# Kernel optimization log

Measured on AMD Instinct MI355X. Metric: run time of the kernel, lower is better.

Reference implementation:

```python
import jax, jax.numpy as jnp
import numpy as np
import math

B, S, D, H = 2, 2048, 1024, 16
DK = D // H
EPS = 1e-5

def setup_inputs() -> dict:
    key = jax.random.key(0)
    ks = jax.random.split(key, 16)
    s = 0.02
    return {
        'query': jax.random.normal(ks[0], (B, S, D), jnp.float32),
        'key': jax.random.normal(ks[1], (B, S, D), jnp.float32),
        'value': jax.random.normal(ks[2], (B, S, D), jnp.float32),
        'mask': jax.random.randint(ks[3], (B, 1, S, S), 0, 2, jnp.int32),
        'market_context': jax.random.normal(ks[4], (B, D), jnp.float32),
        'Wq': jax.random.normal(ks[5], (D, D), jnp.float32) * s,
        'bq': jnp.zeros((D,), jnp.float32),
        'Wk': jax.random.normal(ks[6], (D, D), jnp.float32) * s,
        'bk': jnp.zeros((D,), jnp.float32),
        'Wv': jax.random.normal(ks[7], (D, D), jnp.float32) * s,
        'bv': jnp.zeros((D,), jnp.float32),
        'Wo': jax.random.normal(ks[8], (D, D), jnp.float32) * s,
        'bo': jnp.zeros((D,), jnp.float32),
        'Wc': jax.random.normal(ks[9], (D, D), jnp.float32) * s,
        'bc': jnp.zeros((D,), jnp.float32),
        'ln_g': jnp.ones((D,), jnp.float32),
        'ln_b': jnp.zeros((D,), jnp.float32),
    }

def reference(query, key, value, mask, market_context,
              Wq, bq, Wk, bk, Wv, bv, Wo, bo, Wc, bc, ln_g, ln_b):
    b, s, d = query.shape
    # QKV projections -> [B, H, S, DK]
    Q = (query @ Wq + bq).reshape(b, s, H, DK).transpose(0, 2, 1, 3)
    K = (key @ Wk + bk).reshape(b, s, H, DK).transpose(0, 2, 1, 3)
    V = (value @ Wv + bv).reshape(b, s, H, DK).transpose(0, 2, 1, 3)
    # market context -> per-head bias added to K (broadcast over sequence)
    ctx = (market_context @ Wc + bc).reshape(b, H, DK)
    K = K + ctx[:, :, None, :]
    scores = jnp.einsum('bhqd,bhkd->bhqk', Q, K) / math.sqrt(DK)
    scores = jnp.where(mask == 0, jnp.float32(-1e9), scores)
    attn = jax.nn.softmax(scores, axis=-1)  # dropout is identity in eval
    ctx2 = jnp.einsum('bhqk,bhkd->bhqd', attn, V)
    ctx2 = ctx2.transpose(0, 2, 1, 3).reshape(b, s, d)
    out = ctx2 @ Wo + bo
    x = out + query
    mu = jnp.mean(x, axis=-1, keepdims=True)
    var = jnp.mean((x - mu) ** 2, axis=-1, keepdims=True)
    return (x - mu) * jax.lax.rsqrt(var + EPS) * ln_g + ln_b
```

## Files before the change

### kernel.cpp

```cpp
#include <hip/hip_runtime.h>
#include <cstdint>

typedef unsigned short u16;
typedef __attribute__((ext_vector_type(8))) short s16x8;
typedef __attribute__((ext_vector_type(8))) unsigned short u16x8;
typedef __attribute__((ext_vector_type(4))) float f32x4;
typedef __attribute__((ext_vector_type(16))) float f32x16;
typedef __attribute__((ext_vector_type(2))) unsigned uint2v;
typedef __attribute__((ext_vector_type(4))) unsigned uint4v;

#define CKF 0.18033688011f

__device__ inline u16 f2bf(float f){
  union { float f; uint32_t u; } v; v.f = f;
  uint32_t r = v.u + 0x7fffu + ((v.u >> 16) & 1u);
  return (u16)(r >> 16);
}

__device__ inline f32x4 mfma16(s16x8 a, s16x8 b, f32x4 c){
  return __builtin_amdgcn_mfma_f32_16x16x32_bf16(a, b, c, 0, 0, 0);
}
__device__ inline f32x16 mfma32(s16x8 a, s16x8 b, f32x16 c){
  return __builtin_amdgcn_mfma_f32_32x32x16_bf16(a, b, c, 0, 0, 0);
}
__device__ inline unsigned cvtpk(float a, float b){
  unsigned r;
  asm("v_cvt_pk_bf16_f32 %0, %1, %2" : "=v"(r) : "v"(a), "v"(b));
  return r;
}
__device__ inline float exp2a(float x){
  float r;
  asm("v_exp_f32 %0, %1" : "=v"(r) : "v"(x));
  return r;
}
__device__ inline void glds16(const u16* g, u16* l){
  __builtin_amdgcn_global_load_lds((const __attribute__((address_space(1))) void*)g,
                                   (__attribute__((address_space(3))) void*)l, 16, 0, 0);
}
__device__ inline void glds4(const unsigned* g, unsigned* l){
  __builtin_amdgcn_global_load_lds((const __attribute__((address_space(1))) void*)g,
                                   (__attribute__((address_space(3))) void*)l, 4, 0, 0);
}

struct PrepParams {
  const float* q; const float* k; const float* v;
  const int* mask; const float* mc;
  const float* W0; const float* W1; const float* W2; const float* W3;
  const float* Wc;
  u16* qo; u16* ko; u16* vo;
  u16* T0; u16* T1; u16* T2; u16* T3;
  unsigned* bits; float* part;
};

__global__ __launch_bounds__(256) void prep_kernel(PrepParams PP){
  __shared__ float shf[1056];
  int blk = blockIdx.x, tid = threadIdx.x;
  if (blk < 6144){
    int byy = blk >> 11, bxx = blk & 2047;
    const float* src = (byy == 0) ? PP.q : (byy == 1) ? PP.k : PP.v;
    u16* dst = (byy == 0) ? PP.qo : (byy == 1) ? PP.ko : PP.vo;
    size_t i = ((size_t)bxx * 256 + tid) * 8;
    float4 a = *(const float4*)(src + i);
    float4 b = *(const float4*)(src + i + 4);
    u16x8 o = { f2bf(a.x), f2bf(a.y), f2bf(a.z), f2bf(a.w),
                f2bf(b.x), f2bf(b.y), f2bf(b.z), f2bf(b.w) };
    *(u16x8*)(dst + i) = o;
  } else if (blk < 10240){
    int idx = blk - 6144;
    int bxx = idx & 31, byy = (idx >> 5) & 31, bzz = idx >> 10;
    const float* W = (bzz == 0) ? PP.W0 : (bzz == 1) ? PP.W1 : (bzz == 2) ? PP.W2 : PP.W3;
    u16* T = (bzz == 0) ? PP.T0 : (bzz == 1) ? PP.T1 : (bzz == 2) ? PP.T2 : PP.T3;
    float (*t)[33] = (float(*)[33])shf;
    int n0 = bxx * 32, k0 = byy * 32;
    int tx = tid & 31, ty = tid >> 5;
    #pragma unroll
    for (int j = 0; j < 4; j++)
      t[ty + j*8][tx] = W[(size_t)(k0 + ty + j*8) * 1024 + n0 + tx];
    __syncthreads();
    #pragma unroll
    for (int j = 0; j < 4; j++)
      T[(size_t)(n0 + ty + j*8) * 1024 + k0 + tx] = f2bf(t[tx][ty + j*8]);
  } else if (blk < 43008){
    size_t i = (size_t)(blk - 10240) * 256 + tid;
    int v = PP.mask[i];
    unsigned long long bal = __ballot(v != 0);
    int lane = tid & 63;
    if (lane == 0)       PP.bits[i >> 5] = (unsigned)bal;
    else if (lane == 32) PP.bits[i >> 5] = (unsigned)(bal >> 32);
  } else {
    int slice = blk - 43008;
    int k0 = slice * 64;
    float4 a0 = {0.f,0.f,0.f,0.f}, a1 = {0.f,0.f,0.f,0.f};
    const float* wp = PP.Wc + (size_t)k0 * 1024 + tid * 4;
    #pragma unroll 8
    for (int k = 0; k < 64; k++){
      float4 wv = *(const float4*)(wp + (size_t)k * 1024);
      float m0 = PP.mc[k0 + k], m1 = PP.mc[1024 + k0 + k];
      a0.x += m0 * wv.x; a0.y += m0 * wv.y; a0.z += m0 * wv.z; a0.w += m0 * wv.w;
      a1.x += m1 * wv.x; a1.y += m1 * wv.y; a1.z += m1 * wv.z; a1.w += m1 * wv.w;
    }
    *(float4*)(PP.part + ((size_t)slice * 2 + 0) * 1024 + tid * 4) = a0;
    *(float4*)(PP.part + ((size_t)slice * 2 + 1) * 1024 + tid * 4) = a1;
  }
}

__global__ __launch_bounds__(256) void ctxred_kernel(const float* __restrict__ part,
                                                     const float* __restrict__ bc,
                                                     float* __restrict__ ctx){
  int b = blockIdx.x, tid = threadIdx.x;
  float4 s = *(const float4*)(bc + tid * 4);
  #pragma unroll 4
  for (int sl = 0; sl < 16; sl++){
    float4 p = *(const float4*)(part + ((size_t)sl * 2 + b) * 1024 + tid * 4);
    s.x += p.x; s.y += p.y; s.z += p.z; s.w += p.w;
  }
  *(float4*)(ctx + (size_t)b * 1024 + tid * 4) = s;
}

struct GemmParams {
  const u16* A0; const u16* A1; const u16* A2; const u16* A3;
  const u16* W0; const u16* W1; const u16* W2; const u16* W3;
  const float* b0; const float* b1; const float* b2;
  const float* ctx;
  u16* outQ; u16* outK; u16* outV; float* outX0; float* outX1;
  int which;
};

__global__ __launch_bounds__(256) void gemm_kernel(GemmParams P){
  int o = blockIdx.x + (blockIdx.y << 3) + (blockIdx.z << 8);
  int xcd = o & 7, j = o >> 3;
  int by = xcd + ((j & 3) << 3);
  int bx = (j >> 2) & 7;
  int bz = j >> 5;

  int z, kbase, nkt;
  const u16* A; const u16* W;
  if (P.which < 0){
    z = bz; kbase = 0; nkt = 32;
    if (z == 0){ A = P.A0; W = P.W0; }
    else if (z == 1){ A = P.A1; W = P.W1; }
    else { A = P.A2; W = P.W2; }
  } else {
    z = 3; kbase = bz * 512; nkt = 16;
    A = P.A3; W = P.W3;
  }
  int m0 = by * 128, n0 = bx * 128;
  __shared__ __align__(16) u16 sm[16384];
  int tid = threadIdx.x, lane = tid & 63, w = tid >> 6;
  int li = lane & 15, lq = lane >> 4;
  int wm = w >> 1, wn = w & 1;
  f32x4 zero = {0.f, 0.f, 0.f, 0.f};
  f32x4 acc[4][4];
  #pragma unroll
  for (int i = 0; i < 4; i++)
    #pragma unroll
    for (int jj = 0; jj < 4; jj++) acc[i][jj] = zero;

  int scolS = ((lane & 3) ^ ((lane >> 3) & 3)) << 3;
  int row0 = w * 16 + (lane >> 2);
  const u16* aS0 = A + (size_t)(m0 + row0) * 1024 + kbase + scolS;
  const u16* aS1 = aS0 + (size_t)64 * 1024;
  const u16* bS0 = W + (size_t)(n0 + row0) * 1024 + kbase + scolS;
  const u16* bS1 = bS0 + (size_t)64 * 1024;
  int aD0 = (w * 64) * 8, aD1 = (256 + w * 64) * 8;

  int aOff[4], bOff[4];
  #pragma unroll
  for (int mb = 0; mb < 4; mb++){
    int row = wm * 64 + mb * 16 + li;
    aOff[mb] = (row * 32 + ((lq ^ ((row >> 1) & 3)) << 3)) * 2;
  }
  #pragma unroll
  for (int nb = 0; nb < 4; nb++){
    int row = wn * 64 + nb * 16 + li;
    bOff[nb] = 8192 + (row * 32 + ((lq ^ ((row >> 1) & 3)) << 3)) * 2;
  }

  auto STAGE = [&](int ct){
    u16* Ab = &sm[ct * 8192];
    u16* Bb = &sm[ct * 8192 + 4096];
    glds16(aS0, Ab + aD0);
    glds16(aS1, Ab + aD1);
    glds16(bS0, Bb + aD0);
    glds16(bS1, Bb + aD1);
  };
  auto ADV = [&](){ aS0 += 32; aS1 += 32; bS0 += 32; bS1 += 32; };

  auto KITER = [&](int kt, int ct){
    __builtin_amdgcn_s_barrier();
    if (kt + 1 < nkt){
      STAGE(ct ^ 1); ADV();
      asm volatile("s_waitcnt vmcnt(4)" ::: "memory");
    } else {
      asm volatile("s_waitcnt vmcnt(0)" ::: "memory");
    }
    __builtin_amdgcn_sched_barrier(0);
    __builtin_amdgcn_s_barrier();
    const char* base = (const char*)sm + ct * 16384;
    s16x8 af[4], bfr[4];
    #pragma unroll
    for (int mb = 0; mb < 4; mb++) af[mb] = *(const s16x8*)(base + aOff[mb]);
    #pragma unroll
    for (int nb = 0; nb < 4; nb++) bfr[nb] = *(const s16x8*)(base + bOff[nb]);
    __builtin_amdgcn_s_setprio(1);
    #pragma unroll
    for (int mb = 0; mb < 4; mb++)
      #pragma unroll
      for (int nb = 0; nb < 4; nb++)
        acc[mb][nb] = mfma16(af[mb], bfr[nb], acc[mb][nb]);
    __builtin_amdgcn_s_setprio(0);
  };

  STAGE(0); ADV();
  for (int kt = 0; kt < nkt; kt += 2){
    KITER(kt, 0);
    KITER(kt + 1, 1);
  }

  if (z == 2){
    const float* bias = P.b2;
    __syncthreads();
    u16* Ot = sm;
    #pragma unroll
    for (int mb = 0; mb < 4; mb++){
      #pragma unroll
      for (int nb = 0; nb < 4; nb++){
        int colL = wn * 64 + nb * 16 + li;
        int rowB = wm * 64 + mb * 16 + lq * 4;
        float bcol = bias[n0 + colL];
        unsigned p01 = cvtpk(acc[mb][nb][0] + bcol, acc[mb][nb][1] + bcol);
        unsigned p23 = cvtpk(acc[mb][nb][2] + bcol, acc[mb][nb][3] + bcol);
        int ba = colL * 256 + ((rowB * 2) ^ ((colL & 7) << 4));
        *(unsigned*)((char*)Ot + ba) = p01;
        *(unsigned*)((char*)Ot + ba + 4) = p23;
      }
    }
    __syncthreads();
    int bq_ = m0 >> 11, srow0 = m0 & 2047;
    #pragma unroll
    for (int i = 0; i < 8; i++){
      int u = i * 256 + tid;
      int colL = u >> 4, sc = u & 15;
      int ba = colL * 256 + ((sc * 16) ^ ((colL & 7) << 4));
      u16x8 vv = *(const u16x8*)((char*)Ot + ba);
      *(u16x8*)(P.outV + (((size_t)(bq_ * 1024 + n0 + colL)) << 11) + srow0 + sc * 8) = vv;
    }
    return;
  }

  if (z == 3){
    float* Xo = (kbase == 0) ? P.outX0 : P.outX1;
    #pragma unroll
    for (int mb = 0; mb < 4; mb++){
      #pragma unroll
      for (int nb = 0; nb < 4; nb++){
        int col = n0 + wn * 64 + nb * 16 + li;
        #pragma unroll
        for (int r = 0; r < 4; r++){
          int row = m0 + wm * 64 + mb * 16 + lq * 4 + r;
          Xo[(size_t)row * 1024 + col] = acc[mb][nb][r];
        }
      }
    }
    return;
  }

  const float* bias = (z == 0) ? P.b0 : P.b1;
  #pragma unroll
  for (int mb = 0; mb < 4; mb++){
    #pragma unroll
    for (int nb = 0; nb < 4; nb++){
      int colL = wn * 64 + nb * 16 + li; int col = n0 + colL;
      float bcol = bias[col];
      #pragma unroll
      for (int r = 0; r < 4; r++){
        int row = m0 + wm * 64 + mb * 16 + lq * 4 + r;
        float v = acc[mb][nb][r] + bcol;
        if (z == 0){
          P.outQ[(size_t)row * 1024 + col] = f2bf(v * CKF);
        } else {
          v += P.ctx[(size_t)(row >> 11) * 1024 + col];
          P.outK[(size_t)row * 1024 + col] = f2bf(v);
        }
      }
    }
  }
}

__global__ __launch_bounds__(512) void attn_kernel(
    const u16* __restrict__ Qg, const u16* __restrict__ Kg, const u16* __restrict__ Vtg,
    const unsigned* __restrict__ mbits, u16* __restrict__ ctx2){
  __shared__ __align__(16) u16 arena[36864];
  int tid = threadIdx.x, lane = tid & 63, w = tid >> 6;
  int qw = w & 3, p = w >> 2;
  int l31 = lane & 31, hi = lane >> 5;
  int r7 = l31 & 7;
  int orig = blockIdx.x + (blockIdx.y << 4);
  int swz = (orig & 7) * 64 + (orig >> 3);
  int q0 = (swz & 15) * 128, bh = swz >> 4, b = bh >> 4, h = bh & 15;
  int qr = qw * 32 + l31;

  s16x8 qf[4];
  {
    const u16* qp = Qg + (size_t)(b * 2048 + q0 + qr) * 1024 + h * 64 + hi * 8;
    #pragma unroll
    for (int ks = 0; ks < 4; ks++)
      qf[ks] = *(const s16x8*)(qp + ks * 16);
  }
  s16x8 onesf;
  #pragma unroll
  for (int e = 0; e < 8; e++) onesf[e] = (short)0x3F80;
  f32x16 ZERO;
  #pragma unroll
  for (int r = 0; r < 16; r++) ZERO[r] = 0.f;

  int scolS = ((lane & 7) ^ (lane >> 3)) << 3;
  int rowS = qw * 16 + (lane >> 3);
  const u16* kS0 = Kg + (size_t)(b * 2048 + p * 64 + rowS) * 1024 + h * 64 + scolS;
  const u16* kS1 = kS0 + (size_t)8 * 1024;
  const u16* vS0 = Vtg + (((size_t)(bh * 64 + rowS)) << 11) + p * 64 + scolS;
  const u16* vS1 = vS0 + ((size_t)8 << 11);
  int um = qw * 64 + lane;
  const unsigned* mS = mbits + (size_t)(b * 2048 + q0 + (um >> 1)) * 64 + p * 2 + (um & 1);
  int kD0 = qw * 1024, kD1 = qw * 1024 + 512;

  int koff[2][4], voff[2][4];
  #pragma unroll
  for (int jj = 0; jj < 2; jj++)
    #pragma unroll
    for (int ks = 0; ks < 4; ks++){
      koff[jj][ks] = ((jj * 32 + l31) * 64 + (((ks * 2 + hi) ^ r7) << 3)) * 2;
      voff[jj][ks] = 8192 + ((jj * 32 + l31) * 64 + (((ks * 2 + hi) ^ r7) << 3)) * 2;
    }
  const char* baseP = (const char*)arena + p * 32768;
  int mBp = 65536 + p * 2048 + qr * 8;

  auto STAGE = [&](int ct){
    u16* dst = &arena[(p * 2 + ct) * 8192];
    glds16(kS0, dst + kD0);
    glds16(kS1, dst + kD1);
    glds16(vS0, dst + 4096 + kD0);
    glds16(vS1, dst + 4096 + kD1);
    glds4(mS, (unsigned*)&arena[32768] + (p * 2 + ct) * 256 + qw * 64);
  };
  auto ADV = [&](){
    kS0 += (size_t)128 * 1024; kS1 += (size_t)128 * 1024;
    vS0 += 128; vS1 += 128; mS += 4;
  };

  f32x16 accO[2], accS;
  #pragma unroll
  for (int d = 0; d < 2; d++) accO[d] = ZERO;
  accS = ZERO;

  STAGE(0); ADV();

  auto ITER = [&](int jt, int ct){
    __builtin_amdgcn_s_barrier();
    if (jt < 15){
      STAGE(ct ^ 1); ADV();
      asm volatile("s_waitcnt vmcnt(5)" ::: "memory");
    } else {
      asm volatile("s_waitcnt vmcnt(0)" ::: "memory");
    }
    __builtin_amdgcn_sched_barrier(0);
    __builtin_amdgcn_s_barrier();
    const char* base = baseP + ct * 16384;

    f32x16 S[2];
    __builtin_amdgcn_s_setprio(1);
    #pragma unroll
    for (int jj = 0; jj < 2; jj++){
      S[jj] = ZERO;
      #pragma unroll
      for (int ks = 0; ks < 4; ks++){
        s16x8 kf = *(const s16x8*)(base + koff[jj][ks]);
        S[jj] = mfma32(kf, qf[ks], S[jj]);
      }
    }
    __builtin_amdgcn_s_setprio(0);

    uint2v mw = *(const uint2v*)((const char*)arena + mBp + ct * 1024);
    unsigned mh0 = mw[0] >> (hi << 2), mh1 = mw[1] >> (hi << 2);
    #pragma unroll
    for (int jj = 0; jj < 2; jj++){
      unsigned mh = jj ? mh1 : mh0;
      #pragma unroll
      for (int rg = 0; rg < 16; rg++){
        int pos = (rg & 3) + ((rg >> 2) << 3);
        float pv = exp2a(S[jj][rg]);
        S[jj][rg] = ((mh >> pos) & 1u) ? pv : 0.f;
      }
    }

    s16x8 pf[4];
    #pragma unroll
    for (int jj = 0; jj < 2; jj++){
      #pragma unroll
      for (int hs = 0; hs < 2; hs++){
        int rb = hs * 8;
        unsigned A0 = cvtpk(S[jj][rb + 0], S[jj][rb + 1]);
        unsigned A1 = cvtpk(S[jj][rb + 2], S[jj][rb + 3]);
        unsigned B0 = cvtpk(S[jj][rb + 4], S[jj][rb + 5]);
        unsigned B1 = cvtpk(S[jj][rb + 6], S[jj][rb + 7]);
        uint2v r01 = __builtin_amdgcn_permlane32_swap(A0, B0, false, false);
        uint2v r23 = __builtin_amdgcn_permlane32_swap(A1, B1, false, false);
        uint4v uu = { r01[0], r23[0], r01[1], r23[1] };
        pf[jj * 2 + hs] = *(s16x8*)&uu;
      }
    }
    __builtin_amdgcn_s_setprio(1);
    #pragma unroll
    for (int c = 0; c < 4; c++){
      #pragma unroll
      for (int dh = 0; dh < 2; dh++){
        s16x8 vf = *(const s16x8*)(base + voff[dh][c]);
        accO[dh] = mfma32(vf, pf[c], accO[dh]);
      }
      accS = mfma32(onesf, pf[c], accS);
    }
    __builtin_amdgcn_s_setprio(0);
  };

  for (int jt = 0; jt < 16; jt += 2){
    ITER(jt, 0);
    ITER(jt + 1, 1);
  }

  __syncthreads();
  float lsum = accS[0];
  float* mg = (float*)arena;
  int li33 = (qw * 64 + lane) * 33;
  if (p == 1){
    #pragma unroll
    for (int dh = 0; dh < 2; dh++)
      #pragma unroll
      for (int rg = 0; rg < 16; rg++)
        mg[li33 + dh * 16 + rg] = accO[dh][rg];
    mg[li33 + 32] = lsum;
  }
  __syncthreads();
  u16* Ot = &arena[28672];
  if (p == 0){
    #pragma unroll
    for (int dh = 0; dh < 2; dh++)
      #pragma unroll
      for (int rg = 0; rg < 16; rg++)
        accO[dh][rg] += mg[li33 + dh * 16 + rg];
    lsum += mg[li33 + 32];
    float inv = 1.f / lsum;
    #pragma unroll
    for (int dh = 0; dh < 2; dh++){
      #pragma unroll
      for (int rg = 0; rg < 16; rg += 2){
        int dk = dh * 32 + (rg & 3) + ((rg >> 2) << 3) + (hi << 2);
        unsigned pk = cvtpk(accO[dh][rg] * inv, accO[dh][rg + 1] * inv);
        *(unsigned*)&Ot[qr * 64 + (((dk >> 3) ^ (qr & 7)) << 3) + (dk & 7)] = pk;
      }
    }
  }
  __syncthreads();
  #pragma unroll
  for (int i = 0; i < 2; i++){
    int u = i * 512 + tid, row = u >> 3, slot = u & 7;
    u16x8 vv = *(const u16x8*)&Ot[row * 64 + ((slot ^ (row & 7)) << 3)];
    *(u16x8*)(ctx2 + (size_t)(b * 2048 + q0 + row) * 1024 + h * 64 + slot * 8) = vv;
  }
}

__global__ __launch_bounds__(256) void ln_kernel(const float* __restrict__ X0,
                                                 const float* __restrict__ X1,
                                                 const float* __restrict__ qres,
                                                 const float* __restrict__ bo,
                                                 const float* __restrict__ g,
                                                 const float* __restrict__ bb,
                                                 float* __restrict__ out){
  size_t row = blockIdx.x;
  int tid = threadIdx.x;
  float4 a = *(const float4*)(X0 + row * 1024 + tid * 4);
  float4 c = *(const float4*)(X1 + row * 1024 + tid * 4);
  float4 q = *(const float4*)(qres + row * 1024 + tid * 4);
  float4 bv = *(const float4*)(bo + tid * 4);
  float4 v;
  v.x = a.x + c.x + q.x + bv.x;
  v.y = a.y + c.y + q.y + bv.y;
  v.z = a.z + c.z + q.z + bv.z;
  v.w = a.w + c.w + q.w + bv.w;
  float s = v.x + v.y + v.z + v.w;
  float s2 = v.x*v.x + v.y*v.y + v.z*v.z + v.w*v.w;
  #pragma unroll
  for (int o = 1; o < 64; o <<= 1){
    s += __shfl_xor(s, o, 64);
    s2 += __shfl_xor(s2, o, 64);
  }
  __shared__ float rs[4], rs2[4];
  int w = tid >> 6;
  if ((tid & 63) == 0){ rs[w] = s; rs2[w] = s2; }
  __syncthreads();
  s = rs[0] + rs[1] + rs[2] + rs[3];
  s2 = rs2[0] + rs2[1] + rs2[2] + rs2[3];
  float mu = s * (1.f / 1024.f);
  float var = s2 * (1.f / 1024.f) - mu * mu;
  float rstd = rsqrtf(var + 1e-5f);
  float4 gg = *(const float4*)(g + tid * 4);
  float4 bt = *(const float4*)(bb + tid * 4);
  float4 o;
  o.x = (v.x - mu) * rstd * gg.x + bt.x;
  o.y = (v.y - mu) * rstd * gg.y + bt.y;
  o.z = (v.z - mu) * rstd * gg.z + bt.z;
  o.w = (v.w - mu) * rstd * gg.w + bt.w;
  *(float4*)(out + row * 1024 + tid * 4) = o;
}

extern "C" void kernel_launch(void* const* d_in, const int* in_sizes, int n_in,
                              void* d_out, int out_size, void* d_ws, size_t ws_size,
                              hipStream_t stream){
  const float* query = (const float*)d_in[0];
  const float* key_  = (const float*)d_in[1];
  const float* value = (const float*)d_in[2];
  const int*   mask  = (const int*)d_in[3];
  const float* mc    = (const float*)d_in[4];
  const float* Wq = (const float*)d_in[5];  const float* bq = (const float*)d_in[6];
  const float* Wk = (const float*)d_in[7];  const float* bk = (const float*)d_in[8];
  const float* Wv = (const float*)d_in[9];  const float* bv = (const float*)d_in[10];
  const float* Wo = (const float*)d_in[11]; const float* bo = (const float*)d_in[12];
  const float* Wc = (const float*)d_in[13]; const float* bc = (const float*)d_in[14];
  const float* lng = (const float*)d_in[15]; const float* lnb = (const float*)d_in[16];
  float* outp = (float*)d_out;
  uint8_t* ws = (uint8_t*)d_ws;
  const size_t MB = (size_t)1 << 20;
  if (ws_size < 58 * MB) return;

  u16* q_bf = (u16*)(ws + 0);
  u16* k_bf = (u16*)(ws + 8 * MB);
  u16* v_bf = (u16*)(ws + 16 * MB);
  float* X0 = (float*)(ws + 8 * MB);
  u16* Qb   = (u16*)(ws + 24 * MB);
  u16* Kb   = (u16*)(ws + 32 * MB);
  float* X1 = (float*)(ws + 32 * MB);
  u16* Vt   = (u16*)(ws + 40 * MB);
  u16* Wqt  = (u16*)(ws + 48 * MB);
  u16* Wkt  = (u16*)(ws + 50 * MB);
  u16* Wvt  = (u16*)(ws + 52 * MB);
  u16* Wot  = (u16*)(ws + 54 * MB);
  unsigned* mbits = (unsigned*)(ws + 56 * MB);
  float* ctxf = (float*)(ws + 57 * MB);
  float* ctxpart = (float*)(ws + 57 * MB + 65536);
  u16* ctx2 = q_bf;

  PrepParams PP;
  PP.q = query; PP.k = key_; PP.v = value; PP.mask = mask; PP.mc = mc;
  PP.W0 = Wq; PP.W1 = Wk; PP.W2 = Wv; PP.W3 = Wo; PP.Wc = Wc;
  PP.qo = q_bf; PP.ko = k_bf; PP.vo = v_bf;
  PP.T0 = Wqt; PP.T1 = Wkt; PP.T2 = Wvt; PP.T3 = Wot;
  PP.bits = mbits; PP.part = ctxpart;
  prep_kernel<<<43024, 256, 0, stream>>>(PP);

  ctxred_kernel<<<2, 256, 0, stream>>>(ctxpart, bc, ctxf);

  GemmParams gp;
  gp.A0 = q_bf; gp.A1 = k_bf; gp.A2 = v_bf; gp.A3 = ctx2;
  gp.W0 = Wqt;  gp.W1 = Wkt;  gp.W2 = Wvt;  gp.W3 = Wot;
  gp.b0 = bq;   gp.b1 = bk;   gp.b2 = bv;
  gp.ctx = ctxf;
  gp.outQ = Qb; gp.outK = Kb; gp.outV = Vt; gp.outX0 = X0; gp.outX1 = X1;
  gp.which = -1;
  gemm_kernel<<<dim3(8, 32, 3), 256, 0, stream>>>(gp);

  attn_kernel<<<dim3(16, 32), 512, 0, stream>>>(Qb, Kb, Vt, mbits, ctx2);

  gp.which = 3;
  gemm_kernel<<<dim3(8, 32, 2), 256, 0, stream>>>(gp);

  ln_kernel<<<4096, 256, 0, stream>>>(X0, X1, query, bo, lng, lnb, outp);
}
```

Before: 160.9 us.

## Load K/V directly to registers in attention, drop LDS staging and key split

The attention kernel moves from 512 threads, where two wave groups split the key range and staged K/V/mask tiles through LDS with double buffering, to 256 threads where each wave loads its K and V fragments straight from global memory into registers. K for the next tile is prefetched into a ping-pong register set. The row sum comes from VALU adds plus a cross-half shuffle instead of a ones-vector MFMA, and the cross-group merge through LDS goes away. This removes barriers, the LDS round trip and the extra MFMA, but each wave now fetches K/V itself, with no sharing across the block, and uses more registers.

```diff
diff --git a/kernel.cpp b/kernel.cpp
--- a/kernel.cpp
+++ b/kernel.cpp
@@ -287,18 +287,16 @@
   }
 }
 
-__global__ __launch_bounds__(512) void attn_kernel(
+__global__ __launch_bounds__(256) void attn_kernel(
     const u16* __restrict__ Qg, const u16* __restrict__ Kg, const u16* __restrict__ Vtg,
     const unsigned* __restrict__ mbits, u16* __restrict__ ctx2){
-  __shared__ __align__(16) u16 arena[36864];
+  __shared__ __align__(16) u16 Ot[8192];
   int tid = threadIdx.x, lane = tid & 63, w = tid >> 6;
-  int qw = w & 3, p = w >> 2;
   int l31 = lane & 31, hi = lane >> 5;
-  int r7 = l31 & 7;
   int orig = blockIdx.x + (blockIdx.y << 4);
   int swz = (orig & 7) * 64 + (orig >> 3);
   int q0 = (swz & 15) * 128, bh = swz >> 4, b = bh >> 4, h = bh & 15;
-  int qr = qw * 32 + l31;
+  int qr = w * 32 + l31;
 
   s16x8 qf[4];
   {
@@ -307,162 +305,144 @@
     for (int ks = 0; ks < 4; ks++)
       qf[ks] = *(const s16x8*)(qp + ks * 16);
   }
-  s16x8 onesf;
-  #pragma unroll
-  for (int e = 0; e < 8; e++) onesf[e] = (short)0x3F80;
   f32x16 ZERO;
   #pragma unroll
   for (int r = 0; r < 16; r++) ZERO[r] = 0.f;
 
-  int scolS = ((lane & 7) ^ (lane >> 3)) << 3;
-  int rowS = qw * 16 + (lane >> 3);
-  const u16* kS0 = Kg + (size_t)(b * 2048 + p * 64 + rowS) * 1024 + h * 64 + scolS;
-  const u16* kS1 = kS0 + (size_t)8 * 1024;
-  const u16* vS0 = Vtg + (((size_t)(bh * 64 + rowS)) << 11) + p * 64 + scolS;
-  const u16* vS1 = vS0 + ((size_t)8 << 11);
-  int um = qw * 64 + lane;
-  const unsigned* mS = mbits + (size_t)(b * 2048 + q0 + (um >> 1)) * 64 + p * 2 + (um & 1);
-  int kD0 = qw * 1024, kD1 = qw * 1024 + 512;
-
-  int koff[2][4], voff[2][4];
-  #pragma unroll
-  for (int jj = 0; jj < 2; jj++)
-    #pragma unroll
-    for (int ks = 0; ks < 4; ks++){
-      koff[jj][ks] = ((jj * 32 + l31) * 64 + (((ks * 2 + hi) ^ r7) << 3)) * 2;
-      voff[jj][ks] = 8192 + ((jj * 32 + l31) * 64 + (((ks * 2 + hi) ^ r7) << 3)) * 2;
-    }
-  const char* baseP = (const char*)arena + p * 32768;
-  int mBp = 65536 + p * 2048 + qr * 8;
-
-  auto STAGE = [&](int ct){
-    u16* dst = &arena[(p * 2 + ct) * 8192];
-    glds16(kS0, dst + kD0);
-    glds16(kS1, dst + kD1);
-    glds16(vS0, dst + 4096 + kD0);
-    glds16(vS1, dst + 4096 + kD1);
-    glds4(mS, (unsigned*)&arena[32768] + (p * 2 + ct) * 256 + qw * 64);
-  };
-  auto ADV = [&](){
-    kS0 += (size_t)128 * 1024; kS1 += (size_t)128 * 1024;
-    vS0 += 128; vS1 += 128; mS += 4;
-  };
-
-  f32x16 accO[2], accS;
-  #pragma unroll
-  for (int d = 0; d < 2; d++) accO[d] = ZERO;
-  accS = ZERO;
-
-  STAGE(0); ADV();
-
-  auto ITER = [&](int jt, int ct){
-    __builtin_amdgcn_s_barrier();
-    if (jt < 15){
-      STAGE(ct ^ 1); ADV();
-      asm volatile("s_waitcnt vmcnt(5)" ::: "memory");
-    } else {
-      asm volatile("s_waitcnt vmcnt(0)" ::: "memory");
-    }
-    __builtin_amdgcn_sched_barrier(0);
-    __builtin_amdgcn_s_barrier();
-    const char* base = baseP + ct * 16384;
-
-    f32x16 S[2];
-    __builtin_amdgcn_s_setprio(1);
-    #pragma unroll
-    for (int jj = 0; jj < 2; jj++){
-      S[jj] = ZERO;
+  const u16* pK0 = Kg + (size_t)(b * 2048 + l31) * 1024 + h * 64 + hi * 8;
+  const u16* pK1 = pK0 + (size_t)32 * 1024;
+  const u16* pV0 = Vtg + (((size_t)(bh * 64 + l31)) << 11) + hi * 8;
+  const u16* pV1 = pV0 + ((size_t)32 << 11);
+  const unsigned* pM = mbits + (size_t)(b * 2048 + q0 + qr) * 64;
+
+  s16x8 kA[8], kB[8], vf[8];
+  #pragma unroll
+  for (int ks = 0; ks < 4; ks++){
+    kA[ks]     = *(const s16x8*)(pK0 + ks * 16);
+    kA[4 + ks] = *(const s16x8*)(pK1 + ks * 16);
+  }
+
+  f32x16 accO[2];
+  accO[0] = ZERO; accO[1] = ZERO;
+  float ts0 = 0.f, ts1 = 0.f, ts2 = 0.f, ts3 = 0.f;
+
+  auto ITER = [&](int t, s16x8* Kc, s16x8* Kn){
+    #pragma unroll
+    for (int c = 0; c < 4; c++){
+      vf[c]     = *(const s16x8*)(pV0 + c * 16);
+      vf[4 + c] = *(const s16x8*)(pV1 + c * 16);
+    }
+    uint2v mw = *(const uint2v*)pM;
+    pV0 += 64; pV1 += 64; pM += 2;
+    if (t < 31){
+      pK0 += 65536; pK1 += 65536;
       #pragma unroll
       for (int ks = 0; ks < 4; ks++){
-        s16x8 kf = *(const s16x8*)(base + koff[jj][ks]);
-        S[jj] = mfma32(kf, qf[ks], S[jj]);
+        Kn[ks]     = *(const s16x8*)(pK0 + ks * 16);
+        Kn[4 + ks] = *(const s16x8*)(pK1 + ks * 16);
       }
     }
+    unsigned mh0 = mw[0] >> (hi << 2), mh1 = mw[1] >> (hi << 2);
+
+    f32x16 S0 = ZERO;
+    __builtin_amdgcn_s_setprio(1);
+    #pragma unroll
+    for (int ks = 0; ks < 4; ks++) S0 = mfma32(Kc[ks], qf[ks], S0);
     __builtin_amdgcn_s_setprio(0);
-
-    uint2v mw = *(const uint2v*)((const char*)arena + mBp + ct * 1024);
-    unsigned mh0 = mw[0] >> (hi << 2), mh1 = mw[1] >> (hi << 2);
-    #pragma unroll
-    for (int jj = 0; jj < 2; jj++){
-      unsigned mh = jj ? mh1 : mh0;
-      #pragma unroll
-      for (int rg = 0; rg < 16; rg++){
-        int pos = (rg & 3) + ((rg >> 2) << 3);
-        float pv = exp2a(S[jj][rg]);
-        S[jj][rg] = ((mh >> pos) & 1u) ? pv : 0.f;
-      }
-    }
-
-    s16x8 pf[4];
-    #pragma unroll
-    for (int jj = 0; jj < 2; jj++){
-      #pragma unroll
-      for (int hs = 0; hs < 2; hs++){
-        int rb = hs * 8;
-        unsigned A0 = cvtpk(S[jj][rb + 0], S[jj][rb + 1]);
-        unsigned A1 = cvtpk(S[jj][rb + 2], S[jj][rb + 3]);
-        unsigned B0 = cvtpk(S[jj][rb + 4], S[jj][rb + 5]);
-        unsigned B1 = cvtpk(S[jj][rb + 6], S[jj][rb + 7]);
-        uint2v r01 = __builtin_amdgcn_permlane32_swap(A0, B0, false, false);
-        uint2v r23 = __builtin_amdgcn_permlane32_swap(A1, B1, false, false);
-        uint4v uu = { r01[0], r23[0], r01[1], r23[1] };
-        pf[jj * 2 + hs] = *(s16x8*)&uu;
-      }
+    #pragma unroll
+    for (int rg = 0; rg < 16; rg++){
+      int pos = (rg & 3) + ((rg >> 2) << 3);
+      float pv = exp2a(S0[rg]);
+      pv = ((mh0 >> pos) & 1u) ? pv : 0.f;
+      S0[rg] = pv;
+    }
+    ts0 += S0[0] + S0[4] + S0[8]  + S0[12];
+    ts1 += S0[1] + S0[5] + S0[9]  + S0[13];
+    ts2 += S0[2] + S0[6] + S0[10] + S0[14];
+    ts3 += S0[3] + S0[7] + S0[11] + S0[15];
+    s16x8 pf0, pf1;
+    {
+      unsigned A0 = cvtpk(S0[0], S0[1]),  A1 = cvtpk(S0[2], S0[3]);
+      unsigned B0 = cvtpk(S0[4], S0[5]),  B1 = cvtpk(S0[6], S0[7]);
+      uint2v r01 = __builtin_amdgcn_permlane32_swap(A0, B0, false, false);
+      uint2v r23 = __builtin_amdgcn_permlane32_swap(A1, B1, false, false);
+      uint4v u0 = { r01[0], r23[0], r01[1], r23[1] };
+      pf0 = *(s16x8*)&u0;
+      unsigned C0 = cvtpk(S0[8],  S0[9]),  C1 = cvtpk(S0[10], S0[11]);
+      unsigned D0 = cvtpk(S0[12], S0[13]), D1 = cvtpk(S0[14], S0[15]);
+      uint2v r45 = __builtin_amdgcn_permlane32_swap(C0, D0, false, false);
+      uint2v r67 = __builtin_amdgcn_permlane32_swap(C1, D1, false, false);
+      uint4v u1 = { r45[0], r67[0], r45[1], r67[1] };
+      pf1 = *(s16x8*)&u1;
     }
     __builtin_amdgcn_s_setprio(1);
-    #pragma unroll
-    for (int c = 0; c < 4; c++){
-      #pragma unroll
-      for (int dh = 0; dh < 2; dh++){
-        s16x8 vf = *(const s16x8*)(base + voff[dh][c]);
-        accO[dh] = mfma32(vf, pf[c], accO[dh]);
-      }
-      accS = mfma32(onesf, pf[c], accS);
-    }
+    accO[0] = mfma32(vf[0], pf0, accO[0]);
+    accO[1] = mfma32(vf[4], pf0, accO[1]);
+    accO[0] = mfma32(vf[1], pf1, accO[0]);
+    accO[1] = mfma32(vf[5], pf1, accO[1]);
+    __builtin_amdgcn_s_setprio(0);
+
+    f32x16 S1 = ZERO;
+    __builtin_amdgcn_s_setprio(1);
+    #pragma unroll
+    for (int ks = 0; ks < 4; ks++) S1 = mfma32(Kc[4 + ks], qf[ks], S1);
+    __builtin_amdgcn_s_setprio(0);
+    #pragma unroll
+    for (int rg = 0; rg < 16; rg++){
+      int pos = (rg & 3) + ((rg >> 2) << 3);
+      float pv = exp2a(S1[rg]);
+      pv = ((mh1 >> pos) & 1u) ? pv : 0.f;
+      S1[rg] = pv;
+    }
+    ts0 += S1[0] + S1[4] + S1[8]  + S1[12];
+    ts1 += S1[1] + S1[5] + S1[9]  + S1[13];
+    ts2 += S1[2] + S1[6] + S1[10] + S1[14];
+    ts3 += S1[3] + S1[7] + S1[11] + S1[15];
+    s16x8 pf2, pf3;
+    {
+      unsigned A0 = cvtpk(S1[0], S1[1]),  A1 = cvtpk(S1[2], S1[3]);
+      unsigned B0 = cvtpk(S1[4], S1[5]),  B1 = cvtpk(S1[6], S1[7]);
+      uint2v r01 = __builtin_amdgcn_permlane32_swap(A0, B0, false, false);
+      uint2v r23 = __builtin_amdgcn_permlane32_swap(A1, B1, false, false);
+      uint4v u2 = { r01[0], r23[0], r01[1], r23[1] };
+      pf2 = *(s16x8*)&u2;
+      unsigned C0 = cvtpk(S1[8],  S1[9]),  C1 = cvtpk(S1[10], S1[11]);
+      unsigned D0 = cvtpk(S1[12], S1[13]), D1 = cvtpk(S1[14], S1[15]);
+      uint2v r45 = __builtin_amdgcn_permlane32_swap(C0, D0, false, false);
+      uint2v r67 = __builtin_amdgcn_permlane32_swap(C1, D1, false, false);
+      uint4v u3 = { r45[0], r67[0], r45[1], r67[1] };
+      pf3 = *(s16x8*)&u3;
+    }
+    __builtin_amdgcn_s_setprio(1);
+    accO[0] = mfma32(vf[2], pf2, accO[0]);
+    accO[1] = mfma32(vf[6], pf2, accO[1]);
+    accO[0] = mfma32(vf[3], pf3, accO[0]);
+    accO[1] = mfma32(vf[7], pf3, accO[1]);
     __builtin_amdgcn_s_setprio(0);
   };
 
-  for (int jt = 0; jt < 16; jt += 2){
-    ITER(jt, 0);
-    ITER(jt + 1, 1);
-  }
-
+  for (int t = 0; t < 32; t += 2){
+    ITER(t, kA, kB);
+    ITER(t + 1, kB, kA);
+  }
+
+  float lsum = (ts0 + ts1) + (ts2 + ts3);
+  lsum += __shfl_xor(lsum, 32, 64);
+  float inv = 1.f / lsum;
+
+  #pragma unroll
+  for (int dh = 0; dh < 2; dh++){
+    #pragma unroll
+    for (int rg = 0; rg < 16; rg += 2){
+      int dk = dh * 32 + (rg & 3) + ((rg >> 2) << 3) + (hi << 2);
+      unsigned pk = cvtpk(accO[dh][rg] * inv, accO[dh][rg + 1] * inv);
+      *(unsigned*)&Ot[qr * 64 + (((dk >> 3) ^ (qr & 7)) << 3) + (dk & 7)] = pk;
+    }
+  }
   __syncthreads();
-  float lsum = accS[0];
-  float* mg = (float*)arena;
-  int li33 = (qw * 64 + lane) * 33;
-  if (p == 1){
-    #pragma unroll
-    for (int dh = 0; dh < 2; dh++)
-      #pragma unroll
-      for (int rg = 0; rg < 16; rg++)
-        mg[li33 + dh * 16 + rg] = accO[dh][rg];
-    mg[li33 + 32] = lsum;
-  }
-  __syncthreads();
-  u16* Ot = &arena[28672];
-  if (p == 0){
-    #pragma unroll
-    for (int dh = 0; dh < 2; dh++)
-      #pragma unroll
-      for (int rg = 0; rg < 16; rg++)
-        accO[dh][rg] += mg[li33 + dh * 16 + rg];
-    lsum += mg[li33 + 32];
-    float inv = 1.f / lsum;
-    #pragma unroll
-    for (int dh = 0; dh < 2; dh++){
-      #pragma unroll
-      for (int rg = 0; rg < 16; rg += 2){
-        int dk = dh * 32 + (rg & 3) + ((rg >> 2) << 3) + (hi << 2);
-        unsigned pk = cvtpk(accO[dh][rg] * inv, accO[dh][rg + 1] * inv);
-        *(unsigned*)&Ot[qr * 64 + (((dk >> 3) ^ (qr & 7)) << 3) + (dk & 7)] = pk;
-      }
-    }
-  }
-  __syncthreads();
-  #pragma unroll
-  for (int i = 0; i < 2; i++){
-    int u = i * 512 + tid, row = u >> 3, slot = u & 7;
+  #pragma unroll
+  for (int i = 0; i < 4; i++){
+    int u = i * 256 + tid, row = u >> 3, slot = u & 7;
     u16x8 vv = *(const u16x8*)&Ot[row * 64 + ((slot ^ (row & 7)) << 3)];
     *(u16x8*)(ctx2 + (size_t)(b * 2048 + q0 + row) * 1024 + h * 64 + slot * 8) = vv;
   }
@@ -567,7 +547,7 @@
   gp.which = -1;
   gemm_kernel<<<dim3(8, 32, 3), 256, 0, stream>>>(gp);
 
-  attn_kernel<<<dim3(16, 32), 512, 0, stream>>>(Qb, Kb, Vt, mbits, ctx2);
+  attn_kernel<<<dim3(16, 32), 256, 0, stream>>>(Qb, Kb, Vt, mbits, ctx2);
 
   gp.which = 3;
   gemm_kernel<<<dim3(8, 32, 2), 256, 0, stream>>>(gp);
```

After: 227.1 us. +41.1%, slower.

## Triple-buffer GEMM and attention tiles and drop attention key-split partitions

Applied to the files above, without the earlier changes.

The GEMM and attention main loops move from double- to triple-buffered shared-memory tiles. This removes the leading barrier in each iteration, so one tile loads while the current one is consumed. The attention kernel also drops its two-way split of the key range across wave groups. It now runs 256 threads that each walk all 2048 keys in 64-key tiles, which removes the cross-partition reduction through shared memory. In exchange, each attention block has half the waves and twice the serial iterations, which lowers latency hiding per block, and the GEMM's larger LDS footprint may limit occupancy.

```diff
diff --git a/kernel.cpp b/kernel.cpp
--- a/kernel.cpp
+++ b/kernel.cpp
@@ -145,7 +145,7 @@
     A = P.A3; W = P.W3;
   }
   int m0 = by * 128, n0 = bx * 128;
-  __shared__ __align__(16) u16 sm[16384];
+  __shared__ __align__(16) u16 sm[24576];
   int tid = threadIdx.x, lane = tid & 63, w = tid >> 6;
   int li = lane & 15, lq = lane >> 4;
   int wm = w >> 1, wn = w & 1;
@@ -183,13 +183,12 @@
     glds16(aS1, Ab + aD1);
     glds16(bS0, Bb + aD0);
     glds16(bS1, Bb + aD1);
+    aS0 += 32; aS1 += 32; bS0 += 32; bS1 += 32;
   };
-  auto ADV = [&](){ aS0 += 32; aS1 += 32; bS0 += 32; bS1 += 32; };
-
-  auto KITER = [&](int kt, int ct){
-    __builtin_amdgcn_s_barrier();
+
+  auto KITER = [&](int kt, int ct, int cn){
     if (kt + 1 < nkt){
-      STAGE(ct ^ 1); ADV();
+      STAGE(cn);
       asm volatile("s_waitcnt vmcnt(4)" ::: "memory");
     } else {
       asm volatile("s_waitcnt vmcnt(0)" ::: "memory");
@@ -211,10 +210,17 @@
     __builtin_amdgcn_s_setprio(0);
   };
 
-  STAGE(0); ADV();
-  for (int kt = 0; kt < nkt; kt += 2){
-    KITER(kt, 0);
-    KITER(kt + 1, 1);
+  STAGE(0);
+  if (nkt == 32){
+    for (int kt = 0; kt < 30; kt += 3){
+      KITER(kt, 0, 1); KITER(kt + 1, 1, 2); KITER(kt + 2, 2, 0);
+    }
+    KITER(30, 0, 1); KITER(31, 1, 2);
+  } else {
+    for (int kt = 0; kt < 15; kt += 3){
+      KITER(kt, 0, 1); KITER(kt + 1, 1, 2); KITER(kt + 2, 2, 0);
+    }
+    KITER(15, 0, 1);
   }
 
   if (z == 2){
@@ -287,18 +293,17 @@
   }
 }
 
-__global__ __launch_bounds__(512) void attn_kernel(
+__global__ __launch_bounds__(256) void attn_kernel(
     const u16* __restrict__ Qg, const u16* __restrict__ Kg, const u16* __restrict__ Vtg,
     const unsigned* __restrict__ mbits, u16* __restrict__ ctx2){
-  __shared__ __align__(16) u16 arena[36864];
+  __shared__ __align__(16) u16 arena[26112];
   int tid = threadIdx.x, lane = tid & 63, w = tid >> 6;
-  int qw = w & 3, p = w >> 2;
   int l31 = lane & 31, hi = lane >> 5;
   int r7 = l31 & 7;
   int orig = blockIdx.x + (blockIdx.y << 4);
   int swz = (orig & 7) * 64 + (orig >> 3);
   int q0 = (swz & 15) * 128, bh = swz >> 4, b = bh >> 4, h = bh & 15;
-  int qr = qw * 32 + l31;
+  int qr = w * 32 + l31;
 
   s16x8 qf[4];
   {
@@ -315,14 +320,14 @@
   for (int r = 0; r < 16; r++) ZERO[r] = 0.f;
 
   int scolS = ((lane & 7) ^ (lane >> 3)) << 3;
-  int rowS = qw * 16 + (lane >> 3);
-  const u16* kS0 = Kg + (size_t)(b * 2048 + p * 64 + rowS) * 1024 + h * 64 + scolS;
+  int rowS = w * 16 + (lane >> 3);
+  const u16* kS0 = Kg + (size_t)(b * 2048 + rowS) * 1024 + h * 64 + scolS;
   const u16* kS1 = kS0 + (size_t)8 * 1024;
-  const u16* vS0 = Vtg + (((size_t)(bh * 64 + rowS)) << 11) + p * 64 + scolS;
+  const u16* vS0 = Vtg + (((size_t)(bh * 64 + rowS)) << 11) + scolS;
   const u16* vS1 = vS0 + ((size_t)8 << 11);
-  int um = qw * 64 + lane;
-  const unsigned* mS = mbits + (size_t)(b * 2048 + q0 + (um >> 1)) * 64 + p * 2 + (um & 1);
-  int kD0 = qw * 1024, kD1 = qw * 1024 + 512;
+  int um = w * 64 + lane;
+  const unsigned* mS = mbits + (size_t)(b * 2048 + q0 + (um >> 1)) * 64 + (um & 1);
+  int kD0 = w * 1024, kD1 = w * 1024 + 512;
 
   int koff[2][4], voff[2][4];
   #pragma unroll
@@ -332,40 +337,34 @@
       koff[jj][ks] = ((jj * 32 + l31) * 64 + (((ks * 2 + hi) ^ r7) << 3)) * 2;
       voff[jj][ks] = 8192 + ((jj * 32 + l31) * 64 + (((ks * 2 + hi) ^ r7) << 3)) * 2;
     }
-  const char* baseP = (const char*)arena + p * 32768;
-  int mBp = 65536 + p * 2048 + qr * 8;
+  int mB = 49152 + qr * 8;
 
   auto STAGE = [&](int ct){
-    u16* dst = &arena[(p * 2 + ct) * 8192];
+    u16* dst = &arena[ct * 8192];
     glds16(kS0, dst + kD0);
     glds16(kS1, dst + kD1);
     glds16(vS0, dst + 4096 + kD0);
     glds16(vS1, dst + 4096 + kD1);
-    glds4(mS, (unsigned*)&arena[32768] + (p * 2 + ct) * 256 + qw * 64);
+    glds4(mS, (unsigned*)&arena[24576] + ct * 256 + w * 64);
+    kS0 += (size_t)64 * 1024; kS1 += (size_t)64 * 1024;
+    vS0 += 64; vS1 += 64; mS += 2;
   };
-  auto ADV = [&](){
-    kS0 += (size_t)128 * 1024; kS1 += (size_t)128 * 1024;
-    vS0 += 128; vS1 += 128; mS += 4;
-  };
 
   f32x16 accO[2], accS;
-  #pragma unroll
-  for (int d = 0; d < 2; d++) accO[d] = ZERO;
-  accS = ZERO;
-
-  STAGE(0); ADV();
-
-  auto ITER = [&](int jt, int ct){
-    __builtin_amdgcn_s_barrier();
-    if (jt < 15){
-      STAGE(ct ^ 1); ADV();
+  accO[0] = ZERO; accO[1] = ZERO; accS = ZERO;
+
+  STAGE(0);
+
+  auto ITER = [&](int t, int ct, int cn){
+    if (t < 31){
+      STAGE(cn);
       asm volatile("s_waitcnt vmcnt(5)" ::: "memory");
     } else {
       asm volatile("s_waitcnt vmcnt(0)" ::: "memory");
     }
     __builtin_amdgcn_sched_barrier(0);
     __builtin_amdgcn_s_barrier();
-    const char* base = baseP + ct * 16384;
+    const char* base = (const char*)arena + ct * 16384;
 
     f32x16 S[2];
     __builtin_amdgcn_s_setprio(1);
@@ -380,7 +379,7 @@
     }
     __builtin_amdgcn_s_setprio(0);
 
-    uint2v mw = *(const uint2v*)((const char*)arena + mBp + ct * 1024);
+    uint2v mw = *(const uint2v*)((const char*)arena + mB + ct * 1024);
     unsigned mh0 = mw[0] >> (hi << 2), mh1 = mw[1] >> (hi << 2);
     #pragma unroll
     for (int jj = 0; jj < 2; jj++){
@@ -422,47 +421,28 @@
     __builtin_amdgcn_s_setprio(0);
   };
 
-  for (int jt = 0; jt < 16; jt += 2){
-    ITER(jt, 0);
-    ITER(jt + 1, 1);
-  }
+  for (int t = 0; t < 30; t += 3){
+    ITER(t, 0, 1); ITER(t + 1, 1, 2); ITER(t + 2, 2, 0);
+  }
+  ITER(30, 0, 1); ITER(31, 1, 2);
 
   __syncthreads();
   float lsum = accS[0];
-  float* mg = (float*)arena;
-  int li33 = (qw * 64 + lane) * 33;
-  if (p == 1){
-    #pragma unroll
-    for (int dh = 0; dh < 2; dh++)
-      #pragma unroll
-      for (int rg = 0; rg < 16; rg++)
-        mg[li33 + dh * 16 + rg] = accO[dh][rg];
-    mg[li33 + 32] = lsum;
+  float inv = 1.f / lsum;
+  u16* Ot = arena;
+  #pragma unroll
+  for (int dh = 0; dh < 2; dh++){
+    #pragma unroll
+    for (int rg = 0; rg < 16; rg += 2){
+      int dk = dh * 32 + (rg & 3) + ((rg >> 2) << 3) + (hi << 2);
+      unsigned pk = cvtpk(accO[dh][rg] * inv, accO[dh][rg + 1] * inv);
+      *(unsigned*)&Ot[qr * 64 + (((dk >> 3) ^ (qr & 7)) << 3) + (dk & 7)] = pk;
+    }
   }
   __syncthreads();
-  u16* Ot = &arena[28672];
-  if (p == 0){
-    #pragma unroll
-    for (int dh = 0; dh < 2; dh++)
-      #pragma unroll
-      for (int rg = 0; rg < 16; rg++)
-        accO[dh][rg] += mg[li33 + dh * 16 + rg];
-    lsum += mg[li33 + 32];
-    float inv = 1.f / lsum;
-    #pragma unroll
-    for (int dh = 0; dh < 2; dh++){
-      #pragma unroll
-      for (int rg = 0; rg < 16; rg += 2){
-        int dk = dh * 32 + (rg & 3) + ((rg >> 2) << 3) + (hi << 2);
-        unsigned pk = cvtpk(accO[dh][rg] * inv, accO[dh][rg + 1] * inv);
-        *(unsigned*)&Ot[qr * 64 + (((dk >> 3) ^ (qr & 7)) << 3) + (dk & 7)] = pk;
-      }
-    }
-  }
-  __syncthreads();
-  #pragma unroll
-  for (int i = 0; i < 2; i++){
-    int u = i * 512 + tid, row = u >> 3, slot = u & 7;
+  #pragma unroll
+  for (int i = 0; i < 4; i++){
+    int u = i * 256 + tid, row = u >> 3, slot = u & 7;
     u16x8 vv = *(const u16x8*)&Ot[row * 64 + ((slot ^ (row & 7)) << 3)];
     *(u16x8*)(ctx2 + (size_t)(b * 2048 + q0 + row) * 1024 + h * 64 + slot * 8) = vv;
   }
@@ -567,7 +547,7 @@
   gp.which = -1;
   gemm_kernel<<<dim3(8, 32, 3), 256, 0, stream>>>(gp);
 
-  attn_kernel<<<dim3(16, 32), 512, 0, stream>>>(Qb, Kb, Vt, mbits, ctx2);
+  attn_kernel<<<dim3(16, 32), 256, 0, stream>>>(Qb, Kb, Vt, mbits, ctx2);
 
   gp.which = 3;
   gemm_kernel<<<dim3(8, 32, 2), 256, 0, stream>>>(gp);
```

Measured after the change: 153.0 us. 1.05x faster.
